# Kernel tuning notes

Measured on AMD Instinct MI355X. Metric: run time of the kernel, lower is better.

## Reference

```python
import jax, jax.numpy as jnp
import numpy as np
from jax import lax

KAPPA = 0.01
BC_POWER = 1.5
DX = 1.0 / 2048
ALPHA = 0.5
N_FRAC = 9
GAMMA_1P5 = 0.8862269254527580  # gamma(2 - 0.5)

LAPL = jnp.array([[0.34520446044393, 0.309591078922457, 0.34520446044393],
                  [0.309591078922457, -2.619182157203629, 0.309591078922457],
                  [0.34520446044393, 0.309591078922457, 0.34520446044393]],
                 dtype=jnp.float32)


def _frac_matrix(T, n=N_FRAC, alpha=ALPHA, dt_fixed=0.1):
    # L1-scheme weights: w_0 = 1, w_j = (j+1)^(1-a) - j^(1-a)
    w = np.empty(n + 1, dtype=np.float64)
    w[0] = 1.0
    j = np.arange(1, n + 1, dtype=np.float64)
    w[1:] = (j + 1.0) ** (1.0 - alpha) - j ** (1.0 - alpha)
    M = np.zeros((T, T), dtype=np.float64)  # row 0 stays zero (b starts as zeros)
    for i in range(1, T):
        M[i, i] = w[0]
        M[i, 0] -= w[i - 1]
        for k in range(1, i):
            M[i, k] = -(w[i - k - 1] - w[i - k])
    pref = dt_fixed ** (-alpha) / GAMMA_1P5
    return jnp.asarray(pref * M, dtype=jnp.float32)


def _forward(output, f1):
    u = output[:, 0:1, :, :]           # [T,1,H,W]
    T, _, H, W = u.shape
    # --- phy loss ---
    M = _frac_matrix(T)
    D = jnp.einsum('ts,schw->tchw', M, u)           # fractional time derivative
    lap = lax.conv_general_dilated(u, LAPL[None, None], (1, 1), 'VALID') / (DX ** 2)
    fu = D[:, :, 1:-1, 1:-1] - KAPPA * lap + u[:, :, 1:-1, 1:-1] - f1[:, :, 1:-1, 1:-1]
    phy = 2.0 * jnp.mean(fu * fu)                   # mse(fu,0) + mse(fu,0)
    # --- BC loss ---
    ub = u[1:]                                      # [T-1,1,H,W]
    x = jnp.linspace(0.0, 1.0, W, dtype=u.dtype)
    t = jnp.linspace(0.1, 1.0, T - 1, dtype=u.dtype)
    X, Tm = jnp.meshgrid(x, t, indexing='xy')       # both [T-1, W]
    x1_b = (Tm ** BC_POWER * jnp.sin(2.0 * jnp.pi * X))[:, None, :]  # [T-1,1,W]
    bc = jnp.mean((ub[:, :, :, 0] - x1_b) ** 2
                  + (ub[:, :, :, -1] - x1_b) ** 2
                  + (ub[:, :, 0, :] - x1_b) ** 2
                  + (ub[:, :, -1, :] - x1_b) ** 2) / W
    return phy, bc


def setup_inputs() -> dict:
    key = jax.random.key(0)
    k1, k2 = jax.random.split(key)
    T, H, W = 11, 2048, 2048
    output = jax.random.normal(k1, (T, 1, H, W), dtype=jnp.float32)
    f1 = jax.random.normal(k2, (T, 1, H, W), dtype=jnp.float32)
    return {"output": output, "f1": f1}


def reference(output, f1):
    phy, bc = _forward(output, f1)
    return phy, bc
```

## Files before the change

kernel.cpp:

```cpp
#include <hip/hip_runtime.h>
#include <math.h>

#define HH 2048
#define WW 2048
#define TT 11
constexpr long long HW = (long long)HH * WW;

struct MMat { float m[TT][TT]; };

__device__ __forceinline__ float4 ld4(const float* p) { return *(const float4*)p; }

__global__ __launch_bounds__(256, 4) void phy_kernel(const float* __restrict__ u,
                                                     const float* __restrict__ f1,
                                                     MMat M,
                                                     float* __restrict__ ws)
{
    const int lane = threadIdx.x;
    const int ty   = threadIdx.y;
    const int bx   = blockIdx.x;
    int w0 = bx * 252; if (w0 > WW - 256) w0 = WW - 256;
    const int lo = bx * 252 + 1;
    int hi = bx * 252 + 252; if (hi > WW - 2) hi = WW - 2;

    const int h    = 1 + blockIdx.y * 4 + ty;
    const int heff = (h > HH - 2) ? (HH - 2) : h;
    const float rowmask = (h <= HH - 2) ? 1.0f : 0.0f;

    const int col0 = w0 + lane * 4;
    float4 mask;
    {
        int c0 = col0, c1 = col0 + 1, c2 = col0 + 2, c3 = col0 + 3;
        mask.x = (c0 >= lo && c0 <= hi) ? rowmask : 0.0f;
        mask.y = (c1 >= lo && c1 <= hi) ? rowmask : 0.0f;
        mask.z = (c2 >= lo && c2 <= hi) ? rowmask : 0.0f;
        mask.w = (c3 >= lo && c3 <= hi) ? rowmask : 0.0f;
    }

    const long long rowm = (long long)(heff - 1) * WW + col0;
    const long long row0 = (long long)heff * WW + col0;
    const long long rowp = (long long)(heff + 1) * WW + col0;

    const float c0f = 0.34520446044393f;
    const float c1f = 0.309591078922457f;
    const float c2f = -2.619182157203629f;
    const float kod = 0.01f * 4194304.0f;

    float4 D[TT];
    #pragma unroll
    for (int t = 0; t < TT; ++t) D[t] = make_float4(0.f, 0.f, 0.f, 0.f);

    float acc = 0.0f;

    float4 vm_n = ld4(u + rowm);
    float4 v0_n = ld4(u + row0);
    float4 vp_n = ld4(u + rowp);
    float4 fv_n = ld4(f1 + row0);

    #pragma unroll
    for (int s = 0; s < TT; ++s) {
        const float4 vm = vm_n;
        const float4 v0 = v0_n;
        const float4 vp = vp_n;
        const float4 fv = fv_n;

        if (s + 1 < TT) {
            const float* un = u + (long long)(s + 1) * HW;
            vm_n = ld4(un + rowm);
            v0_n = ld4(un + row0);
            vp_n = ld4(un + rowp);
            fv_n = ld4(f1 + (long long)(s + 1) * HW + row0);
        }

        const float lm = __shfl_up(vm.w, 1);
        const float l0 = __shfl_up(v0.w, 1);
        const float lp = __shfl_up(vp.w, 1);
        const float rm = __shfl_down(vm.x, 1);
        const float r0 = __shfl_down(v0.x, 1);
        const float rp = __shfl_down(vp.x, 1);

        float4 lap;
        lap.x = c0f * ((lm   + vm.y) + (lp   + vp.y)) + c1f * ((vm.x + vp.x) + (l0   + v0.y)) + c2f * v0.x;
        lap.y = c0f * ((vm.x + vm.z) + (vp.x + vp.z)) + c1f * ((vm.y + vp.y) + (v0.x + v0.z)) + c2f * v0.y;
        lap.z = c0f * ((vm.y + vm.w) + (vp.y + vp.w)) + c1f * ((vm.z + vp.z) + (v0.y + v0.w)) + c2f * v0.z;
        lap.w = c0f * ((vm.z + rm  ) + (vp.z + rp  )) + c1f * ((vm.w + vp.w) + (v0.z + r0  )) + c2f * v0.w;

        const float mss = M.m[s][s];
        float fx = (D[s].x + mss * v0.x + (v0.x - kod * lap.x - fv.x)) * mask.x;
        float fy = (D[s].y + mss * v0.y + (v0.y - kod * lap.y - fv.y)) * mask.y;
        float fz = (D[s].z + mss * v0.z + (v0.z - kod * lap.z - fv.z)) * mask.z;
        float fw = (D[s].w + mss * v0.w + (v0.w - kod * lap.w - fv.w)) * mask.w;
        acc += fx * fx + fy * fy + fz * fz + fw * fw;

        #pragma unroll
        for (int t = s + 1; t < TT; ++t) {
            const float m = M.m[t][s];
            D[t].x += m * v0.x;
            D[t].y += m * v0.y;
            D[t].z += m * v0.z;
            D[t].w += m * v0.w;
        }
    }

    #pragma unroll
    for (int off = 32; off > 0; off >>= 1)
        acc += __shfl_down(acc, off, 64);
    __shared__ float wsum[4];
    const int tid = ty * 64 + lane;
    const int wid = tid >> 6;
    if (lane == 0) wsum[wid] = acc;
    __syncthreads();
    if (tid == 0) {
        float s = (wsum[0] + wsum[1]) + (wsum[2] + wsum[3]);
        atomicAdd(&ws[0], s);
    }
}

__global__ __launch_bounds__(256) void bc_kernel(const float* __restrict__ u,
                                                 float* __restrict__ ws)
{
    int idx = blockIdx.x * 256 + threadIdx.x;
    float acc = 0.0f;
    if (idx < 10 * 2048) {
        int i = idx >> 11;
        int j = idx & 2047;
        float tval = 0.1f + 0.1f * (float)i;
        float xj = (float)j * (1.0f / 2047.0f);
        float x1 = powf(tval, 1.5f) * sinf(6.283185307179586f * xj);
        const float* ub = u + (long long)(i + 1) * HW;
        float l = ub[(long long)j * WW + 0]        - x1;
        float r = ub[(long long)j * WW + (WW - 1)] - x1;
        float tp = ub[j]                            - x1;
        float bt = ub[(long long)(HH - 1) * WW + j] - x1;
        acc = l * l + r * r + tp * tp + bt * bt;
    }
    #pragma unroll
    for (int off = 32; off > 0; off >>= 1)
        acc += __shfl_down(acc, off, 64);
    __shared__ float wsum[4];
    int tid = threadIdx.x;
    int lane = tid & 63, wid = tid >> 6;
    if (lane == 0) wsum[wid] = acc;
    __syncthreads();
    if (tid == 0) {
        float s = (wsum[0] + wsum[1]) + (wsum[2] + wsum[3]);
        atomicAdd(&ws[1], s);
    }
}

__global__ void fin_kernel(const float* __restrict__ ws, float* __restrict__ out)
{
    out[0] = ws[0] * (2.0f / (11.0f * 2046.0f * 2046.0f));
    out[1] = ws[1] * (1.0f / (10.0f * 2048.0f * 2048.0f));
}

static MMat make_M()
{
    double w[10];
    w[0] = 1.0;
    for (int j = 1; j <= 9; ++j)
        w[j] = pow((double)j + 1.0, 0.5) - pow((double)j, 0.5);
    double M[TT][TT] = {};
    for (int i = 1; i < TT; ++i) {
        M[i][i] = w[0];
        M[i][0] -= w[i - 1];
        for (int k = 1; k < i; ++k)
            M[i][k] = -(w[i - k - 1] - w[i - k]);
    }
    double pref = pow(0.1, -0.5) / 0.886226925452758;
    MMat r;
    for (int i = 0; i < TT; ++i)
        for (int j = 0; j < TT; ++j)
            r.m[i][j] = (float)(pref * M[i][j]);
    return r;
}

extern "C" void kernel_launch(void* const* d_in, const int* in_sizes, int n_in,
                              void* d_out, int out_size, void* d_ws, size_t ws_size,
                              hipStream_t stream)
{
    const float* u  = (const float*)d_in[0];
    const float* f1 = (const float*)d_in[1];
    float* out = (float*)d_out;
    float* ws  = (float*)d_ws;

    MMat M = make_M();

    hipMemsetAsync(ws, 0, 2 * sizeof(float), stream);

    dim3 block(64, 4);
    dim3 grid(9, 512);
    phy_kernel<<<grid, block, 0, stream>>>(u, f1, M, ws);

    bc_kernel<<<(10 * 2048 + 255) / 256, 256, 0, stream>>>(u, ws);

    fin_kernel<<<1, 1, 0, stream>>>(ws, out);
}
```

Measured before the change: 372.8 us.

## Stage stencil rows through LDS with direct global-to-LDS loads

Each block now loads the six u rows and four f1 rows it needs for a time step into a double-buffered shared-memory tile, using the global_load_lds builtin with 16-byte transfers. The four waves then read their stencil rows from LDS instead of each loading three overlapping u rows from global memory. This removes the redundant halo-row loads across waves and moves data straight into LDS without passing through registers. The cost is a block-wide barrier every time step and 20 KB of shared memory per block, which can reduce occupancy and serialize the waves.

```diff
diff --git a/kernel.cpp b/kernel.cpp
--- a/kernel.cpp
+++ b/kernel.cpp
@@ -8,7 +8,13 @@
 
 struct MMat { float m[TT][TT]; };
 
-__device__ __forceinline__ float4 ld4(const float* p) { return *(const float4*)p; }
+__device__ __forceinline__ void gload_lds16(const float* g, float* l)
+{
+    __builtin_amdgcn_global_load_lds(
+        (const __attribute__((address_space(1))) unsigned int*)g,
+        (__attribute__((address_space(3))) unsigned int*)l,
+        16, 0, 0);
+}
 
 __global__ __launch_bounds__(256, 4) void phy_kernel(const float* __restrict__ u,
                                                      const float* __restrict__ f1,
@@ -22,8 +28,8 @@
     const int lo = bx * 252 + 1;
     int hi = bx * 252 + 252; if (hi > WW - 2) hi = WW - 2;
 
-    const int h    = 1 + blockIdx.y * 4 + ty;
-    const int heff = (h > HH - 2) ? (HH - 2) : h;
+    const int h0 = 1 + blockIdx.y * 4;
+    const int h  = h0 + ty;
     const float rowmask = (h <= HH - 2) ? 1.0f : 0.0f;
 
     const int col0 = w0 + lane * 4;
@@ -36,9 +42,13 @@
         mask.w = (c3 >= lo && c3 <= hi) ? rowmask : 0.0f;
     }
 
-    const long long rowm = (long long)(heff - 1) * WW + col0;
-    const long long row0 = (long long)heff * WW + col0;
-    const long long rowp = (long long)(heff + 1) * WW + col0;
+    int urow[6], frow[4];
+    #pragma unroll
+    for (int r = 0; r < 6; ++r) { int g = h0 - 1 + r; urow[r] = (g > HH - 1) ? (HH - 1) : g; }
+    #pragma unroll
+    for (int r = 0; r < 4; ++r) { int g = h0 + r;     frow[r] = (g > HH - 1) ? (HH - 1) : g; }
+
+    __shared__ float lds[2][10 * 256];
 
     const float c0f = 0.34520446044393f;
     const float c1f = 0.309591078922457f;
@@ -51,25 +61,31 @@
 
     float acc = 0.0f;
 
-    float4 vm_n = ld4(u + rowm);
-    float4 v0_n = ld4(u + row0);
-    float4 vp_n = ld4(u + rowp);
-    float4 fv_n = ld4(f1 + row0);
+    auto stageRow = [&](int s, int b, int r) {
+        const float* base = (r < 6)
+            ? (u  + (long long)s * HW + (long long)urow[r]     * WW)
+            : (f1 + (long long)s * HW + (long long)frow[r - 6] * WW);
+        gload_lds16(base + w0 + lane * 4, &lds[b][r * 256]);
+    };
+    auto stage = [&](int s, int b) {
+        stageRow(s, b, ty);
+        stageRow(s, b, ty + 4);
+        if (ty < 2) stageRow(s, b, ty + 8);
+    };
+
+    stage(0, 0);
 
     #pragma unroll
     for (int s = 0; s < TT; ++s) {
-        const float4 vm = vm_n;
-        const float4 v0 = v0_n;
-        const float4 vp = vp_n;
-        const float4 fv = fv_n;
-
-        if (s + 1 < TT) {
-            const float* un = u + (long long)(s + 1) * HW;
-            vm_n = ld4(un + rowm);
-            v0_n = ld4(un + row0);
-            vp_n = ld4(un + rowp);
-            fv_n = ld4(f1 + (long long)(s + 1) * HW + row0);
-        }
+        __syncthreads();
+
+        if (s + 1 < TT) stage(s + 1, (s + 1) & 1);
+
+        const float* Lb = &lds[s & 1][0];
+        const float4 vm = *(const float4*)&Lb[(ty    ) * 256 + lane * 4];
+        const float4 v0 = *(const float4*)&Lb[(ty + 1) * 256 + lane * 4];
+        const float4 vp = *(const float4*)&Lb[(ty + 2) * 256 + lane * 4];
+        const float4 fv = *(const float4*)&Lb[(6 + ty) * 256 + lane * 4];
 
         const float lm = __shfl_up(vm.w, 1);
         const float l0 = __shfl_up(v0.w, 1);
```

Result: slower. 545.6 us (+46.3%).
